# Performance work log

Hardware: AMD Instinct MI355X
Metric: run time of the kernel (lower is better)

## Reference

```python
import jax, jax.numpy as jnp
import numpy as np

H = 16            # num heads
D_NOPE = 128
D_ROPE = 64
D_V = 128
Q_LORA = 1536
KV_LORA = 512
HIDDEN = 2048
EPS = 1e-6


def rmsnorm(x, w):
    xf = x.astype(jnp.float32)
    var = jnp.mean(xf * xf, axis=-1, keepdims=True)
    return (w * (xf * jax.lax.rsqrt(var + EPS))).astype(x.dtype)


def rope_interleaved(x, cos, sin):
    # x: [B,H,S,D]; cos,sin: [S,D] -> use even-index entries as the per-pair values
    B, nH, S, D = x.shape
    cv = cos[:, 0::2].astype(jnp.float32)[None, None]  # [1,1,S,D/2]
    sv = sin[:, 0::2].astype(jnp.float32)[None, None]
    xf = x.astype(jnp.float32).reshape(B, nH, S, D // 2, 2)
    xr, xi = xf[..., 0], xf[..., 1]
    out = jnp.stack([xr * cv - xi * sv, xr * sv + xi * cv], axis=-1)
    return out.reshape(B, nH, S, D).astype(x.dtype)


def setup_inputs() -> dict:
    key = jax.random.key(0)
    ks = jax.random.split(key, 9)
    B, S = 2, 2048
    std = 0.02
    return {
        "hidden_states": jax.random.normal(ks[0], (B, S, HIDDEN), jnp.float32),
        "cos": jax.random.uniform(ks[1], (S, D_ROPE), jnp.float32),
        "sin": jax.random.uniform(ks[2], (S, D_ROPE), jnp.float32),
        "q_a_w": jax.random.normal(ks[3], (HIDDEN, Q_LORA), jnp.float32) * std,
        "q_a_ln_w": jnp.ones((Q_LORA,), jnp.float32),
        "q_b_w": jax.random.normal(ks[4], (Q_LORA, H * (D_NOPE + D_ROPE)), jnp.float32) * std,
        "kv_a_w": jax.random.normal(ks[5], (HIDDEN, KV_LORA + D_ROPE), jnp.float32) * std,
        "kv_a_ln_w": jnp.ones((KV_LORA,), jnp.float32),
        "kv_b_w": jax.random.normal(ks[6], (KV_LORA, H * (D_NOPE + D_V)), jnp.float32) * std,
        "o_w": jax.random.normal(ks[7], (H * D_V, HIDDEN), jnp.float32) * std,
    }


def reference(hidden_states, cos, sin, q_a_w, q_a_ln_w, q_b_w, kv_a_w, kv_a_ln_w, kv_b_w, o_w):
    B, S, _ = hidden_states.shape
    scale = 1.0 / np.sqrt(D_NOPE + D_ROPE)

    # Q path: low-rank down-proj, RMSNorm, up-proj
    q = rmsnorm(hidden_states @ q_a_w, q_a_ln_w) @ q_b_w
    q = q.reshape(B, S, H, D_NOPE + D_ROPE).transpose(0, 2, 1, 3)  # [B,H,S,Dq]
    q_nope, q_rope = q[..., :D_NOPE], q[..., D_NOPE:]

    # KV path: compressed kv + shared rope key
    ckv = hidden_states @ kv_a_w  # [B,S,KV_LORA+D_ROPE]
    compressed_kv, k_rope = ckv[..., :KV_LORA], ckv[..., KV_LORA:]
    k_rope = jnp.broadcast_to(k_rope[:, None], (B, H, S, D_ROPE))
    kv = rmsnorm(compressed_kv, kv_a_ln_w) @ kv_b_w
    kv = kv.reshape(B, S, H, D_NOPE + D_V).transpose(0, 2, 1, 3)  # [B,H,S,Dk+Dv]
    k_nope, value = kv[..., :D_NOPE], kv[..., D_NOPE:]

    q_rope = rope_interleaved(q_rope, cos, sin)
    k_rope = rope_interleaved(k_rope, cos, sin)

    query = jnp.concatenate([q_nope, q_rope], axis=-1)  # [B,H,S,192]
    key = jnp.concatenate([k_nope, k_rope], axis=-1)

    attn = jnp.einsum("bhqd,bhkd->bhqk", query, key) * scale
    attn = jax.nn.softmax(attn.astype(jnp.float32), axis=-1).astype(query.dtype)
    out = jnp.einsum("bhqk,bhkd->bhqd", attn, value)  # [B,H,S,Dv]
    out = out.transpose(0, 2, 1, 3).reshape(B, S, H * D_V)
    return out @ o_w
```

## Files before the change

kernel.cpp:

```cpp
#include <hip/hip_runtime.h>

typedef unsigned short u16;
typedef __bf16 bf16x8 __attribute__((ext_vector_type(8)));
typedef float f32x4 __attribute__((ext_vector_type(4)));
typedef u16 u16x4 __attribute__((ext_vector_type(4)));

#define S_ 2048

__device__ __forceinline__ u16 f2bf(float f) {
  union { float f; unsigned u; } v; v.f = f;
  unsigned r = v.u + 0x7fffu + ((v.u >> 16) & 1u);
  return (u16)(r >> 16);
}

__device__ __forceinline__ f32x4 mfma16(bf16x8 a, bf16x8 b, f32x4 c) {
  return __builtin_amdgcn_mfma_f32_16x16x32_bf16(a, b, c, 0, 0, 0);
}

__device__ __forceinline__ void async16(const void* g, void* l) {
  __builtin_amdgcn_global_load_lds((__attribute__((address_space(1))) void*)g,
                                   (__attribute__((address_space(3))) void*)l,
                                   16, 0, 0);
}

#define QSCALE2 0.10411756755f

__global__ __launch_bounds__(256)
void prep_k(const float* __restrict__ hs, u16* __restrict__ hs_bf,
            const float* __restrict__ q_a_w, const float* __restrict__ kv_a_w,
            const float* __restrict__ q_b_w, const float* __restrict__ kv_b_w,
            const float* __restrict__ o_w,
            u16* __restrict__ qakvT, u16* __restrict__ qbwT,
            u16* __restrict__ kvbwT, u16* __restrict__ owT) {
  int blk = blockIdx.x;
  int tid = threadIdx.x;
  if (blk < 4096) {
    int i = blk * 256 + tid;
    f32x4 a = ((const f32x4*)hs)[2 * i], b = ((const f32x4*)hs)[2 * i + 1];
    union { u16 v[8]; f32x4 q; } u;
#pragma unroll
    for (int e = 0; e < 4; ++e) { u.v[e] = f2bf(a[e]); u.v[4 + e] = f2bf(b[e]); }
    ((f32x4*)hs_bf)[i] = u.q;
    return;
  }
  blk -= 4096;
  const float* W; u16* Wt; int K, N, gx;
  if (blk < 3072)       { W = q_a_w;  Wt = qakvT;                     K = 2048; N = 1536; gx = 64; }
  else if (blk < 4352)  { blk -= 3072;  W = kv_a_w; Wt = qakvT + (long)1536 * 2048; K = 2048; N = 576;  gx = 64; }
  else if (blk < 8960)  { blk -= 4352;  W = q_b_w;  Wt = qbwT;  K = 1536; N = 3072; gx = 48; }
  else if (blk < 11008) { blk -= 8960;  W = kv_b_w; Wt = kvbwT; K = 512;  N = 4096; gx = 16; }
  else                  { blk -= 11008; W = o_w;    Wt = owT;   K = 2048; N = 2048; gx = 64; }
  int k0 = (blk % gx) * 32, n0 = (blk / gx) * 32;
  int tx = tid & 31, ty = tid >> 5;
  __shared__ float tile[32][33];
#pragma unroll
  for (int r = 0; r < 32; r += 8) {
    int n = n0 + tx;
    tile[ty + r][tx] = (n < N) ? W[(long)(k0 + ty + r) * N + n] : 0.f;
  }
  __syncthreads();
#pragma unroll
  for (int r = 0; r < 32; r += 8) {
    Wt[(long)(n0 + ty + r) * K + k0 + tx] = f2bf(tile[tx][ty + r]);
  }
}

__device__ __forceinline__ int xcd_chunk(int lin, int nwg) {
  if ((nwg & 7) == 0) return (lin & 7) * (nwg >> 3) + (lin >> 3);
  return lin;
}

template <typename OUT_T, bool ROPE>
__global__ __launch_bounds__(256)
void gemm_bt_k(const u16* __restrict__ A, const u16* __restrict__ Bt,
               OUT_T* __restrict__ C, int K, int Nc, int ldc,
               const float* __restrict__ cs, const float* __restrict__ sn) {
  __shared__ __align__(16) u16 sA[2][128 * 32];
  __shared__ __align__(16) u16 sB[2][128 * 32];
  int tid = threadIdx.x;
  int lane = tid & 63, w = tid >> 6;
  int wr = w >> 1, wc = w & 1;
  int l15 = lane & 15, quad = lane >> 4;
  int gx = gridDim.x;
  int nl = xcd_chunk(blockIdx.x + gx * blockIdx.y, gx * gridDim.y);
  long tm = (long)(nl / gx) * 128;
  long tn = (long)(nl % gx) * 128;
  const u16* Ab = A + tm * K;
  const u16* Bb = Bt + tn * K;
  f32x4 acc[4][4] = {};

#pragma unroll
  for (int it = 0; it < 2; ++it) {
    int c = tid + it * 256;
    int row = c >> 2, sl = c & 3;
    int kc = sl ^ ((row >> 1) & 3);
    async16(Ab + (long)row * K + kc * 8, &sA[0][c * 8]);
    async16(Bb + (long)row * K + kc * 8, &sB[0][c * 8]);
  }

  int nk = K >> 5;
  for (int kt = 0; kt < nk; ++kt) {
    int cur = kt & 1;
    __syncthreads();
    if (kt + 1 < nk) {
      int k0n = (kt + 1) << 5;
#pragma unroll
      for (int it = 0; it < 2; ++it) {
        int c = tid + it * 256;
        int row = c >> 2, sl = c & 3;
        int kc = sl ^ ((row >> 1) & 3);
        async16(Ab + (long)row * K + k0n + kc * 8, &sA[cur ^ 1][c * 8]);
        async16(Bb + (long)row * K + k0n + kc * 8, &sB[cur ^ 1][c * 8]);
      }
    }
    bf16x8 af[4], bfr[4];
#pragma unroll
    for (int i = 0; i < 4; ++i) {
      int rowa = wr * 64 + i * 16 + l15;
      int slot = quad ^ ((rowa >> 1) & 3);
      af[i] = *(const bf16x8*)(&sA[cur][(rowa * 4 + slot) * 8]);
    }
#pragma unroll
    for (int j = 0; j < 4; ++j) {
      int rowb = wc * 64 + j * 16 + l15;
      int slot = quad ^ ((rowb >> 1) & 3);
      bfr[j] = *(const bf16x8*)(&sB[cur][(rowb * 4 + slot) * 8]);
    }
#pragma unroll
    for (int i = 0; i < 4; ++i)
#pragma unroll
      for (int j = 0; j < 4; ++j)
        acc[i][j] = mfma16(af[i], bfr[j], acc[i][j]);
  }
#pragma unroll
  for (int i = 0; i < 4; ++i) {
#pragma unroll
    for (int j = 0; j < 4; ++j) {
      int col = (int)tn + wc * 64 + j * 16 + l15;
      if (col < Nc) {
        bool ropeT = false;
        int fi = 0;
        if constexpr (ROPE) {
          int d = col % 192;
          ropeT = (d >= 128);
          fi = (d - 128) & ~1;
        }
#pragma unroll
        for (int r = 0; r < 4; ++r) {
          long row = tm + wr * 64 + i * 16 + quad * 4 + r;
          float v = acc[i][j][r];
          if constexpr (ROPE) {
            float partner = __shfl_xor(v, 1);
            if (ropeT) {
              int si = (int)row & (S_ - 1);
              float cv = cs[si * 64 + fi], sv = sn[si * 64 + fi];
              v = (l15 & 1) ? (partner * sv + v * cv)
                            : (v * cv - partner * sv);
            }
            v *= QSCALE2;
          }
          if constexpr (sizeof(OUT_T) == 2) C[row * ldc + col] = f2bf(v);
          else                              C[row * ldc + col] = v;
        }
      }
    }
  }
}

__global__ __launch_bounds__(256)
void gemm_kvb_k(const u16* __restrict__ A, const u16* __restrict__ Bt,
                u16* __restrict__ kswz, u16* __restrict__ vswz,
                const u16* __restrict__ kr) {
  const int K = 512;
  __shared__ __align__(16) u16 sA[2][128 * 32];
  __shared__ __align__(16) u16 sB[2][128 * 32];
  int tid = threadIdx.x;
  int lane = tid & 63, w = tid >> 6;
  int wr = w >> 1, wc = w & 1;
  int l15 = lane & 15, quad = lane >> 4;
  int gx = gridDim.x;
  int nl = xcd_chunk(blockIdx.x + gx * blockIdx.y, gx * gridDim.y);
  long tm = (long)(nl / gx) * 128;
  long tn = (long)(nl % gx) * 128;
  const u16* Ab = A + tm * K;
  const u16* Bb = Bt + tn * K;
  f32x4 acc[4][4] = {};

#pragma unroll
  for (int it = 0; it < 2; ++it) {
    int c = tid + it * 256;
    int row = c >> 2, sl = c & 3;
    int kc = sl ^ ((row >> 1) & 3);
    async16(Ab + (long)row * K + kc * 8, &sA[0][c * 8]);
    async16(Bb + (long)row * K + kc * 8, &sB[0][c * 8]);
  }

  const int nk = K >> 5;
  for (int kt = 0; kt < nk; ++kt) {
    int cur = kt & 1;
    __syncthreads();
    if (kt + 1 < nk) {
      int k0n = (kt + 1) << 5;
#pragma unroll
      for (int it = 0; it < 2; ++it) {
        int c = tid + it * 256;
        int row = c >> 2, sl = c & 3;
        int kc = sl ^ ((row >> 1) & 3);
        async16(Ab + (long)row * K + k0n + kc * 8, &sA[cur ^ 1][c * 8]);
        async16(Bb + (long)row * K + k0n + kc * 8, &sB[cur ^ 1][c * 8]);
      }
    }
    bf16x8 af[4], bfr[4];
#pragma unroll
    for (int i = 0; i < 4; ++i) {
      int rowa = wr * 64 + i * 16 + l15;
      int slot = quad ^ ((rowa >> 1) & 3);
      af[i] = *(const bf16x8*)(&sA[cur][(rowa * 4 + slot) * 8]);
    }
#pragma unroll
    for (int j = 0; j < 4; ++j) {
      int rowb = wc * 64 + j * 16 + l15;
      int slot = quad ^ ((rowb >> 1) & 3);
      bfr[j] = *(const bf16x8*)(&sB[cur][(rowb * 4 + slot) * 8]);
    }
#pragma unroll
    for (int i = 0; i < 4; ++i)
#pragma unroll
      for (int j = 0; j < 4; ++j)
        acc[i][j] = mfma16(af[i], bfr[j], acc[i][j]);
  }

  int h = (int)(tn >> 8);
  int b = (int)(tm >> 11);
  int kt0 = ((int)tm & 2047) >> 6;
  int tile = (b * 16 + h) * 32 + kt0 + wr;
  if ((tn & 255) == 0) {
    u16* dst = kswz + (long)tile * 12288;
#pragma unroll
    for (int i = 0; i < 4; ++i) {
#pragma unroll
      for (int j = 0; j < 4; ++j) {
        int frag = quad * 6 + wc * 2 + (j >> 1);
        int chunk = frag * 64 + ((j & 1) * 2 + (l15 >> 3)) * 16 + i * 4;
#pragma unroll
        for (int r = 0; r < 4; ++r)
          dst[(chunk + r) * 8 + (l15 & 7)] = f2bf(acc[i][j][r]);
      }
    }
#pragma unroll
    for (int it = 0; it < 4; ++it) {
      int c = tid + it * 256;
      int tt = c >> 9;
      int cc = c & 511;
      int lane2 = cc & 63, fd = cc >> 6;
      int kg = fd >> 1, dbr = fd & 1;
      int sl = lane2 & 15;
      int key = (kt0 + tt) * 64 + (sl >> 2) * 16 + kg * 4 + (sl & 3);
      int doff = dbr * 32 + (lane2 >> 4) * 8;
      int frag = kg * 6 + 4 + dbr;
      u16* dst2 = kswz + (long)((b * 16 + h) * 32 + kt0 + tt) * 12288;
      *(f32x4*)(dst2 + (frag * 64 + lane2) * 8) =
          *(const f32x4*)(kr + ((long)(b * S_ + key)) * 64 + doff);
    }
  } else {
    u16* dst = vswz + (long)tile * 8192;
    int kq = quad >> 1;
    int e0 = (quad & 1) * 4;
#pragma unroll
    for (int i = 0; i < 4; ++i) {
#pragma unroll
      for (int j = 0; j < 4; ++j) {
        int frag = kq * 8 + wc * 4 + j;
        u16x4 pk;
#pragma unroll
        for (int r = 0; r < 4; ++r) pk[r] = f2bf(acc[i][j][r]);
        *(u16x4*)(dst + (frag * 64 + i * 16 + l15) * 8 + e0) = pk;
      }
    }
  }
}

__global__ __launch_bounds__(256)
void rmsnorm2_k(const float* __restrict__ qsrc, int ldq,
                const float* __restrict__ kvsrc, int ldkv,
                const float* __restrict__ wq, const float* __restrict__ wkv,
                u16* __restrict__ qout, u16* __restrict__ kvout,
                const float* __restrict__ cs, const float* __restrict__ sn,
                u16* __restrict__ krout) {
  int blk = blockIdx.x;
  if (blk >= 8192) {
    int idx = (blk - 8192) * 256 + threadIdx.x;
    int row = idx >> 5, i = idx & 31;
    int s = row & (S_ - 1);
    const float* src = qsrc + 2048;
    float xr = src[(long)row * ldq + 2 * i];
    float xi = src[(long)row * ldq + 2 * i + 1];
    float cv = cs[s * 64 + 2 * i], sv = sn[s * 64 + 2 * i];
    krout[(long)row * 64 + 2 * i]     = f2bf(xr * cv - xi * sv);
    krout[(long)row * 64 + 2 * i + 1] = f2bf(xr * sv + xi * cv);
    return;
  }
  const float* x; const float* wt; u16* o; int N;
  if (blk < 4096) { x = qsrc + (long)blk * ldq;  wt = wq;  o = qout + (long)blk * 1536;  N = 1536; }
  else { blk -= 4096; x = kvsrc + (long)blk * ldkv; wt = wkv; o = kvout + (long)blk * 512; N = 512; }
  float ss = 0.f;
  for (int i = threadIdx.x; i < N; i += 256) { float v = x[i]; ss += v * v; }
#pragma unroll
  for (int off = 32; off; off >>= 1) ss += __shfl_down(ss, off);
  __shared__ float red[4];
  if ((threadIdx.x & 63) == 0) red[threadIdx.x >> 6] = ss;
  __syncthreads();
  float inv = rsqrtf((red[0] + red[1] + red[2] + red[3]) / N + 1e-6f);
  for (int i = threadIdx.x; i < N; i += 256) o[i] = f2bf(wt[i] * x[i] * inv);
}

__global__ __launch_bounds__(256, 2)
void attn_k(const u16* __restrict__ qb, const u16* __restrict__ kswz,
            const u16* __restrict__ vswz, u16* __restrict__ attnO) {
  int lin = blockIdx.x + 16 * blockIdx.y;
  int xcd = lin & 7;
  int j = lin >> 3;
  int bh = (xcd << 2) + (j >> 4);
  int qt = j & 15;
  int b = bh >> 4, h = bh & 15;
  int tid = threadIdx.x, lane = tid & 63, w = tid >> 6;
  int l15 = lane & 15, quad = lane >> 4;
  int qrow0 = qt * 128 + w * 32;

  __shared__ __align__(16) u16 sK[2][24 * 64 * 8];

  const u16* Kb = kswz + (long)bh * 32 * 12288;
  const u16* Vb = vswz + (long)bh * 32 * 8192;

  bf16x8 qf[2][6];
#pragma unroll
  for (int rg = 0; rg < 2; ++rg) {
    const u16* qp = qb + ((long)(b * S_ + qrow0 + rg * 16 + l15)) * 3072 + h * 192 + quad * 8;
#pragma unroll
    for (int kb = 0; kb < 6; ++kb) qf[rg][kb] = *(const bf16x8*)(qp + kb * 32);
  }

  union { u16 v[8]; bf16x8 b; } ones;
#pragma unroll
  for (int e = 0; e < 8; ++e) ones.v[e] = 0x3F80;

  f32x4 o[2][8] = {};
  f32x4 lacc[2] = {};

#pragma unroll
  for (int i = 0; i < 6; ++i) { int c = tid + i * 256; async16(Kb + c * 8, &sK[0][c * 8]); }

#pragma unroll 1
  for (int kt = 0; kt < 32; ++kt) {
    int cur = kt & 1;
    __syncthreads();
    if (kt < 31) {
      const u16* Kt = Kb + (long)(kt + 1) * 12288;
#pragma unroll
      for (int i = 0; i < 6; ++i) { int c = tid + i * 256; async16(Kt + c * 8, &sK[cur ^ 1][c * 8]); }
    }

    const u16* kbase = sK[cur];
    const u16* Vt = Vb + (long)kt * 8192;

    bf16x8 vf0[8], vf1[8];
#pragma unroll
    for (int f = 0; f < 8; ++f)
      vf0[f] = *(const bf16x8*)(Vt + (f * 64 + lane) * 8);

    f32x4 s[2][4] = {};
    __builtin_amdgcn_s_setprio(1);
#pragma unroll
    for (int db = 0; db < 6; ++db) {
      bf16x8 kf[4];
#pragma unroll
      for (int kg = 0; kg < 4; ++kg)
        kf[kg] = *(const bf16x8*)(kbase + ((kg * 6 + db) * 64 + lane) * 8);
#pragma unroll
      for (int kg = 0; kg < 4; ++kg) {
        s[0][kg] = mfma16(kf[kg], qf[0][db], s[0][kg]);
        s[1][kg] = mfma16(kf[kg], qf[1][db], s[1][kg]);
      }
    }
    __builtin_amdgcn_s_setprio(0);

#pragma unroll
    for (int f = 0; f < 8; ++f)
      vf1[f] = *(const bf16x8*)(Vt + ((8 + f) * 64 + lane) * 8);

    bf16x8 pf[2][2];
#pragma unroll
    for (int rg = 0; rg < 2; ++rg) {
#pragma unroll
      for (int kg = 0; kg < 4; ++kg) {
#pragma unroll
        for (int r = 0; r < 4; ++r)
          s[rg][kg][r] = __builtin_amdgcn_exp2f(s[rg][kg][r]);
      }
#pragma unroll
      for (int kq = 0; kq < 2; ++kq) {
        union { unsigned wd[4]; bf16x8 v; } u;
        asm("v_cvt_pk_bf16_f32 %0, %1, %2"
            : "=v"(u.wd[0]) : "v"(s[rg][2 * kq][0]), "v"(s[rg][2 * kq][1]));
        asm("v_cvt_pk_bf16_f32 %0, %1, %2"
            : "=v"(u.wd[1]) : "v"(s[rg][2 * kq][2]), "v"(s[rg][2 * kq][3]));
        asm("v_cvt_pk_bf16_f32 %0, %1, %2"
            : "=v"(u.wd[2]) : "v"(s[rg][2 * kq + 1][0]), "v"(s[rg][2 * kq + 1][1]));
        asm("v_cvt_pk_bf16_f32 %0, %1, %2"
            : "=v"(u.wd[3]) : "v"(s[rg][2 * kq + 1][2]), "v"(s[rg][2 * kq + 1][3]));
        pf[rg][kq] = u.v;
      }
      lacc[rg] = mfma16(pf[rg][0], ones.b, lacc[rg]);
      lacc[rg] = mfma16(pf[rg][1], ones.b, lacc[rg]);
    }

    __builtin_amdgcn_s_setprio(1);
#pragma unroll
    for (int j2 = 0; j2 < 8; ++j2) {
      o[0][j2] = mfma16(pf[0][0], vf0[j2], o[0][j2]);
      o[1][j2] = mfma16(pf[1][0], vf0[j2], o[1][j2]);
    }
#pragma unroll
    for (int j2 = 0; j2 < 8; ++j2) {
      o[0][j2] = mfma16(pf[0][1], vf1[j2], o[0][j2]);
      o[1][j2] = mfma16(pf[1][1], vf1[j2], o[1][j2]);
    }
    __builtin_amdgcn_s_setprio(0);
  }

#pragma unroll
  for (int rg = 0; rg < 2; ++rg) {
    u16* op = attnO + ((long)(b * S_ + qrow0 + rg * 16)) * 2048 + h * 128;
    float invr[4];
#pragma unroll
    for (int r = 0; r < 4; ++r) invr[r] = 1.f / lacc[rg][r];
#pragma unroll
    for (int j2 = 0; j2 < 8; ++j2)
#pragma unroll
      for (int r = 0; r < 4; ++r)
        op[(long)(quad * 4 + r) * 2048 + j2 * 16 + l15] = f2bf(o[rg][j2][r] * invr[r]);
  }
}

extern "C" void kernel_launch(void* const* d_in, const int* in_sizes, int n_in,
                              void* d_out, int out_size, void* d_ws, size_t ws_size,
                              hipStream_t stream) {
  const float* hs      = (const float*)d_in[0];
  const float* cosb    = (const float*)d_in[1];
  const float* sinb    = (const float*)d_in[2];
  const float* q_a_w   = (const float*)d_in[3];
  const float* q_a_ln  = (const float*)d_in[4];
  const float* q_b_w   = (const float*)d_in[5];
  const float* kv_a_w  = (const float*)d_in[6];
  const float* kv_a_ln = (const float*)d_in[7];
  const float* kv_b_w  = (const float*)d_in[8];
  const float* o_w     = (const float*)d_in[9];
  float* out = (float*)d_out;
  (void)in_sizes; (void)n_in; (void)out_size; (void)ws_size;

  char* p = (char*)d_ws;
  auto alloc = [&](size_t b) { char* r = p; p += (b + 255) & ~((size_t)255); return r; };
  u16*   hs_bf  = (u16*)  alloc((size_t)4096 * 2048 * 2);
  u16*   qakvT  = (u16*)  alloc((size_t)2176 * 2048 * 2);
  u16*   qbwT   = (u16*)  alloc((size_t)3072 * 1536 * 2);
  u16*   kvbwT  = (u16*)  alloc((size_t)4096 * 512  * 2);
  u16*   owT    = (u16*)  alloc((size_t)2048 * 2048 * 2);
  float* qa_ckv = (float*)alloc((size_t)4096 * 2176 * 4);
  u16*   qan    = (u16*)  alloc((size_t)4096 * 1536 * 2);
  u16*   ckvn   = (u16*)  alloc((size_t)4096 * 512  * 2);
  u16*   kr     = (u16*)  alloc((size_t)4096 * 64   * 2);
  u16*   qbuf   = (u16*)  alloc((size_t)4096 * 3072 * 2);
  u16*   aO     = (u16*)  alloc((size_t)4096 * 2048 * 2);
  u16* kswz = (u16*)qa_ckv;
  u16* vswz = (u16*)hs_bf;

  prep_k<<<19200, 256, 0, stream>>>(hs, hs_bf, q_a_w, kv_a_w, q_b_w, kv_b_w,
                                    o_w, qakvT, qbwT, kvbwT, owT);

  gemm_bt_k<float, false><<<dim3(17, 32), 256, 0, stream>>>(
      hs_bf, qakvT, qa_ckv, 2048, 2176, 2176, nullptr, nullptr);
  rmsnorm2_k<<<8704, 256, 0, stream>>>(qa_ckv, 2176, qa_ckv + 1536, 2176,
                                       q_a_ln, kv_a_ln, qan, ckvn,
                                       cosb, sinb, kr);
  gemm_bt_k<u16, true><<<dim3(24, 32), 256, 0, stream>>>(
      qan, qbwT, qbuf, 1536, 3072, 3072, cosb, sinb);
  gemm_kvb_k<<<dim3(32, 32), 256, 0, stream>>>(ckvn, kvbwT, kswz, vswz, kr);
  attn_k<<<dim3(16, 32), 256, 0, stream>>>(qbuf, kswz, vswz, aO);
  gemm_bt_k<float, false><<<dim3(16, 32), 256, 0, stream>>>(
      aO, owT, out, 2048, 2048, 2048, nullptr, nullptr);
}
```

Baseline: 462.0 us.

## Overlap weight transposes with A-projection GEMM and merge Q/KV up-projections into one launch

Moves the q_b/kv_b/o weight transposes out of the prep kernel and runs them as extra blocks in the same launch as the A-projection GEMM, so the memory-bound transposes can fill idle CUs alongside the compute-bound GEMM. The Q up-projection (with RoPE) and KV up-projection GEMMs are merged into a single launch with the block range split between them. This cuts launch count and tail idleness. The cost is more shared-memory reservation for the transpose blocks and possible contention between GEMM and transpose traffic.

```diff
diff --git a/kernel.cpp b/kernel.cpp
--- a/kernel.cpp
+++ b/kernel.cpp
@@ -25,66 +25,41 @@
 
 #define QSCALE2 0.10411756755f
 
-__global__ __launch_bounds__(256)
-void prep_k(const float* __restrict__ hs, u16* __restrict__ hs_bf,
-            const float* __restrict__ q_a_w, const float* __restrict__ kv_a_w,
-            const float* __restrict__ q_b_w, const float* __restrict__ kv_b_w,
-            const float* __restrict__ o_w,
-            u16* __restrict__ qakvT, u16* __restrict__ qbwT,
-            u16* __restrict__ kvbwT, u16* __restrict__ owT) {
-  int blk = blockIdx.x;
-  int tid = threadIdx.x;
-  if (blk < 4096) {
-    int i = blk * 256 + tid;
-    f32x4 a = ((const f32x4*)hs)[2 * i], b = ((const f32x4*)hs)[2 * i + 1];
-    union { u16 v[8]; f32x4 q; } u;
-#pragma unroll
-    for (int e = 0; e < 4; ++e) { u.v[e] = f2bf(a[e]); u.v[4 + e] = f2bf(b[e]); }
-    ((f32x4*)hs_bf)[i] = u.q;
-    return;
-  }
-  blk -= 4096;
-  const float* W; u16* Wt; int K, N, gx;
-  if (blk < 3072)       { W = q_a_w;  Wt = qakvT;                     K = 2048; N = 1536; gx = 64; }
-  else if (blk < 4352)  { blk -= 3072;  W = kv_a_w; Wt = qakvT + (long)1536 * 2048; K = 2048; N = 576;  gx = 64; }
-  else if (blk < 8960)  { blk -= 4352;  W = q_b_w;  Wt = qbwT;  K = 1536; N = 3072; gx = 48; }
-  else if (blk < 11008) { blk -= 8960;  W = kv_b_w; Wt = kvbwT; K = 512;  N = 4096; gx = 16; }
-  else                  { blk -= 11008; W = o_w;    Wt = owT;   K = 2048; N = 2048; gx = 64; }
-  int k0 = (blk % gx) * 32, n0 = (blk / gx) * 32;
-  int tx = tid & 31, ty = tid >> 5;
-  __shared__ float tile[32][33];
-#pragma unroll
-  for (int r = 0; r < 32; r += 8) {
-    int n = n0 + tx;
-    tile[ty + r][tx] = (n < N) ? W[(long)(k0 + ty + r) * N + n] : 0.f;
-  }
-  __syncthreads();
-#pragma unroll
-  for (int r = 0; r < 32; r += 8) {
-    Wt[(long)(n0 + ty + r) * K + k0 + tx] = f2bf(tile[tx][ty + r]);
-  }
-}
-
 __device__ __forceinline__ int xcd_chunk(int lin, int nwg) {
   if ((nwg & 7) == 0) return (lin & 7) * (nwg >> 3) + (lin >> 3);
   return lin;
 }
 
+__device__ __forceinline__ void transw_body(const float* __restrict__ W,
+                                            u16* __restrict__ Wt, int K, int N,
+                                            int blk, int gx, float* tile) {
+  int tid = threadIdx.x;
+  int k0 = (blk % gx) * 32, n0 = (blk / gx) * 32;
+  int tx = tid & 31, ty = tid >> 5;
+#pragma unroll
+  for (int r = 0; r < 32; r += 8) {
+    int n = n0 + tx;
+    tile[(ty + r) * 33 + tx] = (n < N) ? W[(long)(k0 + ty + r) * N + n] : 0.f;
+  }
+  __syncthreads();
+#pragma unroll
+  for (int r = 0; r < 32; r += 8) {
+    Wt[(long)(n0 + ty + r) * K + k0 + tx] = f2bf(tile[tx * 33 + ty + r]);
+  }
+}
+
 template <typename OUT_T, bool ROPE>
-__global__ __launch_bounds__(256)
-void gemm_bt_k(const u16* __restrict__ A, const u16* __restrict__ Bt,
-               OUT_T* __restrict__ C, int K, int Nc, int ldc,
-               const float* __restrict__ cs, const float* __restrict__ sn) {
-  __shared__ __align__(16) u16 sA[2][128 * 32];
-  __shared__ __align__(16) u16 sB[2][128 * 32];
+__device__ __forceinline__ void gemm_bt_body(
+    const u16* __restrict__ A, const u16* __restrict__ Bt,
+    OUT_T* __restrict__ C, int K, int Nc, int ldc,
+    const float* __restrict__ cs, const float* __restrict__ sn,
+    int nl, int gxT, u16* sAbuf, u16* sBbuf) {
   int tid = threadIdx.x;
   int lane = tid & 63, w = tid >> 6;
   int wr = w >> 1, wc = w & 1;
   int l15 = lane & 15, quad = lane >> 4;
-  int gx = gridDim.x;
-  int nl = xcd_chunk(blockIdx.x + gx * blockIdx.y, gx * gridDim.y);
-  long tm = (long)(nl / gx) * 128;
-  long tn = (long)(nl % gx) * 128;
+  long tm = (long)(nl / gxT) * 128;
+  long tn = (long)(nl % gxT) * 128;
   const u16* Ab = A + tm * K;
   const u16* Bb = Bt + tn * K;
   f32x4 acc[4][4] = {};
@@ -94,8 +69,8 @@
     int c = tid + it * 256;
     int row = c >> 2, sl = c & 3;
     int kc = sl ^ ((row >> 1) & 3);
-    async16(Ab + (long)row * K + kc * 8, &sA[0][c * 8]);
-    async16(Bb + (long)row * K + kc * 8, &sB[0][c * 8]);
+    async16(Ab + (long)row * K + kc * 8, sAbuf + c * 8);
+    async16(Bb + (long)row * K + kc * 8, sBbuf + c * 8);
   }
 
   int nk = K >> 5;
@@ -109,8 +84,8 @@
         int c = tid + it * 256;
         int row = c >> 2, sl = c & 3;
         int kc = sl ^ ((row >> 1) & 3);
-        async16(Ab + (long)row * K + k0n + kc * 8, &sA[cur ^ 1][c * 8]);
-        async16(Bb + (long)row * K + k0n + kc * 8, &sB[cur ^ 1][c * 8]);
+        async16(Ab + (long)row * K + k0n + kc * 8, sAbuf + (cur ^ 1) * 4096 + c * 8);
+        async16(Bb + (long)row * K + k0n + kc * 8, sBbuf + (cur ^ 1) * 4096 + c * 8);
       }
     }
     bf16x8 af[4], bfr[4];
@@ -118,13 +93,13 @@
     for (int i = 0; i < 4; ++i) {
       int rowa = wr * 64 + i * 16 + l15;
       int slot = quad ^ ((rowa >> 1) & 3);
-      af[i] = *(const bf16x8*)(&sA[cur][(rowa * 4 + slot) * 8]);
+      af[i] = *(const bf16x8*)(sAbuf + cur * 4096 + (rowa * 4 + slot) * 8);
     }
 #pragma unroll
     for (int j = 0; j < 4; ++j) {
       int rowb = wc * 64 + j * 16 + l15;
       int slot = quad ^ ((rowb >> 1) & 3);
-      bfr[j] = *(const bf16x8*)(&sB[cur][(rowb * 4 + slot) * 8]);
+      bfr[j] = *(const bf16x8*)(sBbuf + cur * 4096 + (rowb * 4 + slot) * 8);
     }
 #pragma unroll
     for (int i = 0; i < 4; ++i)
@@ -167,21 +142,17 @@
   }
 }
 
-__global__ __launch_bounds__(256)
-void gemm_kvb_k(const u16* __restrict__ A, const u16* __restrict__ Bt,
-                u16* __restrict__ kswz, u16* __restrict__ vswz,
-                const u16* __restrict__ kr) {
+__device__ __forceinline__ void gemm_kvb_body(
+    const u16* __restrict__ A, const u16* __restrict__ Bt,
+    u16* __restrict__ kswz, u16* __restrict__ vswz,
+    const u16* __restrict__ kr, int nl, u16* sAbuf, u16* sBbuf) {
   const int K = 512;
-  __shared__ __align__(16) u16 sA[2][128 * 32];
-  __shared__ __align__(16) u16 sB[2][128 * 32];
   int tid = threadIdx.x;
   int lane = tid & 63, w = tid >> 6;
   int wr = w >> 1, wc = w & 1;
   int l15 = lane & 15, quad = lane >> 4;
-  int gx = gridDim.x;
-  int nl = xcd_chunk(blockIdx.x + gx * blockIdx.y, gx * gridDim.y);
-  long tm = (long)(nl / gx) * 128;
-  long tn = (long)(nl % gx) * 128;
+  long tm = (long)(nl / 32) * 128;
+  long tn = (long)(nl % 32) * 128;
   const u16* Ab = A + tm * K;
   const u16* Bb = Bt + tn * K;
   f32x4 acc[4][4] = {};
@@ -191,8 +162,8 @@
     int c = tid + it * 256;
     int row = c >> 2, sl = c & 3;
     int kc = sl ^ ((row >> 1) & 3);
-    async16(Ab + (long)row * K + kc * 8, &sA[0][c * 8]);
-    async16(Bb + (long)row * K + kc * 8, &sB[0][c * 8]);
+    async16(Ab + (long)row * K + kc * 8, sAbuf + c * 8);
+    async16(Bb + (long)row * K + kc * 8, sBbuf + c * 8);
   }
 
   const int nk = K >> 5;
@@ -206,8 +177,8 @@
         int c = tid + it * 256;
         int row = c >> 2, sl = c & 3;
         int kc = sl ^ ((row >> 1) & 3);
-        async16(Ab + (long)row * K + k0n + kc * 8, &sA[cur ^ 1][c * 8]);
-        async16(Bb + (long)row * K + k0n + kc * 8, &sB[cur ^ 1][c * 8]);
+        async16(Ab + (long)row * K + k0n + kc * 8, sAbuf + (cur ^ 1) * 4096 + c * 8);
+        async16(Bb + (long)row * K + k0n + kc * 8, sBbuf + (cur ^ 1) * 4096 + c * 8);
       }
     }
     bf16x8 af[4], bfr[4];
@@ -215,13 +186,13 @@
     for (int i = 0; i < 4; ++i) {
       int rowa = wr * 64 + i * 16 + l15;
       int slot = quad ^ ((rowa >> 1) & 3);
-      af[i] = *(const bf16x8*)(&sA[cur][(rowa * 4 + slot) * 8]);
+      af[i] = *(const bf16x8*)(sAbuf + cur * 4096 + (rowa * 4 + slot) * 8);
     }
 #pragma unroll
     for (int j = 0; j < 4; ++j) {
       int rowb = wc * 64 + j * 16 + l15;
       int slot = quad ^ ((rowb >> 1) & 3);
-      bfr[j] = *(const bf16x8*)(&sB[cur][(rowb * 4 + slot) * 8]);
+      bfr[j] = *(const bf16x8*)(sBbuf + cur * 4096 + (rowb * 4 + slot) * 8);
     }
 #pragma unroll
     for (int i = 0; i < 4; ++i)
@@ -278,6 +249,84 @@
       }
     }
   }
+}
+
+__global__ __launch_bounds__(256)
+void prep_k(const float* __restrict__ hs, u16* __restrict__ hs_bf,
+            const float* __restrict__ q_a_w, const float* __restrict__ kv_a_w,
+            u16* __restrict__ qakvT) {
+  __shared__ float tile[32 * 33];
+  int blk = blockIdx.x;
+  int tid = threadIdx.x;
+  if (blk < 4096) {
+    int i = blk * 256 + tid;
+    f32x4 a = ((const f32x4*)hs)[2 * i], b = ((const f32x4*)hs)[2 * i + 1];
+    union { u16 v[8]; f32x4 q; } u;
+#pragma unroll
+    for (int e = 0; e < 4; ++e) { u.v[e] = f2bf(a[e]); u.v[4 + e] = f2bf(b[e]); }
+    ((f32x4*)hs_bf)[i] = u.q;
+    return;
+  }
+  blk -= 4096;
+  if (blk < 3072) transw_body(q_a_w, qakvT, 2048, 1536, blk, 64, tile);
+  else            transw_body(kv_a_w, qakvT + (long)1536 * 2048, 2048, 576,
+                              blk - 3072, 64, tile);
+}
+
+__global__ __launch_bounds__(256)
+void aproj_trans_k(const u16* __restrict__ hs_bf, const u16* __restrict__ qakvT,
+                   float* __restrict__ qa_ckv,
+                   const float* __restrict__ q_b_w, const float* __restrict__ kv_b_w,
+                   const float* __restrict__ o_w,
+                   u16* __restrict__ qbwT, u16* __restrict__ kvbwT,
+                   u16* __restrict__ owT) {
+  __shared__ __align__(16) char smem[32768];
+  int lin = blockIdx.x;
+  if (lin < 544) {
+    u16* sAbuf = (u16*)smem;
+    u16* sBbuf = sAbuf + 8192;
+    gemm_bt_body<float, false>(hs_bf, qakvT, qa_ckv, 2048, 2176, 2176,
+                               nullptr, nullptr, xcd_chunk(lin, 544), 17,
+                               sAbuf, sBbuf);
+    return;
+  }
+  float* tile = (float*)smem;
+  int blk = lin - 544;
+  if (blk < 4608)      transw_body(q_b_w,  qbwT,  1536, 3072, blk, 48, tile);
+  else if (blk < 6656) transw_body(kv_b_w, kvbwT, 512,  4096, blk - 4608, 16, tile);
+  else                 transw_body(o_w,    owT,   2048, 2048, blk - 6656, 64, tile);
+}
+
+__global__ __launch_bounds__(256)
+void qbkvb_k(const u16* __restrict__ qan, const u16* __restrict__ qbwT,
+             u16* __restrict__ qbuf,
+             const float* __restrict__ cs, const float* __restrict__ sn,
+             const u16* __restrict__ ckvn, const u16* __restrict__ kvbwT,
+             u16* __restrict__ kswz, u16* __restrict__ vswz,
+             const u16* __restrict__ kr) {
+  __shared__ __align__(16) char smem[32768];
+  u16* sAbuf = (u16*)smem;
+  u16* sBbuf = sAbuf + 8192;
+  int lin = blockIdx.x;
+  if (lin < 768) {
+    gemm_bt_body<u16, true>(qan, qbwT, qbuf, 1536, 3072, 3072, cs, sn,
+                            xcd_chunk(lin, 768), 24, sAbuf, sBbuf);
+  } else {
+    gemm_kvb_body(ckvn, kvbwT, kswz, vswz, kr,
+                  xcd_chunk(lin - 768, 1024), sAbuf, sBbuf);
+  }
+}
+
+template <typename OUT_T, bool ROPE>
+__global__ __launch_bounds__(256)
+void gemm_bt_k(const u16* __restrict__ A, const u16* __restrict__ Bt,
+               OUT_T* __restrict__ C, int K, int Nc, int ldc,
+               const float* __restrict__ cs, const float* __restrict__ sn) {
+  __shared__ __align__(16) u16 sAbuf[2 * 4096];
+  __shared__ __align__(16) u16 sBbuf[2 * 4096];
+  int gx = gridDim.x;
+  int nl = xcd_chunk(blockIdx.x + gx * blockIdx.y, gx * gridDim.y);
+  gemm_bt_body<OUT_T, ROPE>(A, Bt, C, K, Nc, ldc, cs, sn, nl, gx, sAbuf, sBbuf);
 }
 
 __global__ __launch_bounds__(256)
@@ -474,17 +523,15 @@
   u16* kswz = (u16*)qa_ckv;
   u16* vswz = (u16*)hs_bf;
 
-  prep_k<<<19200, 256, 0, stream>>>(hs, hs_bf, q_a_w, kv_a_w, q_b_w, kv_b_w,
-                                    o_w, qakvT, qbwT, kvbwT, owT);
-
-  gemm_bt_k<float, false><<<dim3(17, 32), 256, 0, stream>>>(
-      hs_bf, qakvT, qa_ckv, 2048, 2176, 2176, nullptr, nullptr);
+  prep_k<<<8448, 256, 0, stream>>>(hs, hs_bf, q_a_w, kv_a_w, qakvT);
+  aproj_trans_k<<<11296, 256, 0, stream>>>(hs_bf, qakvT, qa_ckv,
+                                           q_b_w, kv_b_w, o_w,
+                                           qbwT, kvbwT, owT);
   rmsnorm2_k<<<8704, 256, 0, stream>>>(qa_ckv, 2176, qa_ckv + 1536, 2176,
                                        q_a_ln, kv_a_ln, qan, ckvn,
                                        cosb, sinb, kr);
-  gemm_bt_k<u16, true><<<dim3(24, 32), 256, 0, stream>>>(
-      qan, qbwT, qbuf, 1536, 3072, 3072, cosb, sinb);
-  gemm_kvb_k<<<dim3(32, 32), 256, 0, stream>>>(ckvn, kvbwT, kswz, vswz, kr);
+  qbkvb_k<<<1792, 256, 0, stream>>>(qan, qbwT, qbuf, cosb, sinb,
+                                    ckvn, kvbwT, kswz, vswz, kr);
   attn_k<<<dim3(16, 32), 256, 0, stream>>>(qbuf, kswz, vswz, aO);
   gemm_bt_k<float, false><<<dim3(16, 32), 256, 0, stream>>>(
       aO, owT, out, 2048, 2048, 2048, nullptr, nullptr);
```

New measurement: 444.3 us. -3.8%, faster.
